# Kernel optimization log

Measured on AMD Instinct MI355X. Metric: run time of the kernel, lower is better.

## Reference

```python
import jax, jax.numpy as jnp
import numpy as np

B, C_IN, H, W = 8, 32, 64, 64
C = 64  # num_channels


def setup_inputs() -> dict:
    key = jax.random.key(0)
    ks = jax.random.split(key, 9)
    s_in = 1.0 / np.sqrt(C_IN)
    s_c = 1.0 / np.sqrt(C)
    return {
        "x": jax.random.normal(ks[0], (B, C_IN, H, W), dtype=jnp.float32),
        "wq": jax.random.uniform(ks[1], (C, C_IN), jnp.float32, -s_in, s_in),
        "bq": jax.random.uniform(ks[2], (C,), jnp.float32, -s_in, s_in),
        "wk": jax.random.uniform(ks[3], (C, C_IN), jnp.float32, -s_in, s_in),
        "bk": jax.random.uniform(ks[4], (C,), jnp.float32, -s_in, s_in),
        "wv": jax.random.uniform(ks[5], (C, C_IN), jnp.float32, -s_in, s_in),
        "bv": jax.random.uniform(ks[6], (C,), jnp.float32, -s_in, s_in),
        "wo": jax.random.uniform(ks[7], (C_IN, C), jnp.float32, -s_c, s_c),
        "bo": jax.random.uniform(ks[8], (C_IN,), jnp.float32, -s_c, s_c),
    }


def reference(x, wq, bq, wk, bk, wv, bv, wo, bo):
    b, c_in, h, w = x.shape
    n = h * w
    # 1x1 convs == per-pixel linear projections; produce (B, N, C) directly
    q = (jnp.einsum('bchw,oc->bhwo', x, wq) + bq).reshape(b, n, -1)
    k = (jnp.einsum('bchw,oc->bhwo', x, wk) + bk).reshape(b, n, -1)
    v = (jnp.einsum('bchw,oc->bhwo', x, wv) + bv).reshape(b, n, -1)
    # unscaled attention over spatial positions (no 1/sqrt(d) in original)
    scores = jnp.einsum('bnc,bmc->bnm', q, k)  # (B, N, N)
    attn = jax.nn.softmax(scores, axis=-1)
    out = jnp.einsum('bnm,bmc->bnc', attn, v)  # (B, N, C)
    out = out.reshape(b, h, w, -1)
    out = jnp.einsum('bhwc,oc->bohw', out, wo) + bo[None, :, None, None]
    return out + x
```

## Files before the change

### kernel.cpp

```cpp
#include <hip/hip_runtime.h>
#include <hip/hip_bf16.h>

#define CIN    32
#define NPIX   4096
#define DIM    64
#define LOG2E  1.4426950408889634f

#if __has_builtin(__builtin_amdgcn_exp2f)
#define EXP2(x) __builtin_amdgcn_exp2f(x)
#else
#define EXP2(x) exp2f(x)
#endif

typedef float  f32x4 __attribute__((ext_vector_type(4)));
typedef short  s16x8 __attribute__((ext_vector_type(8)));

__device__ __forceinline__ unsigned short bf16_bits(float f) {
    union { __hip_bfloat16 h; unsigned short u; } cv;
    cv.h = __float2bfloat16(f);
    return cv.u;
}


__global__ __launch_bounds__(256) void qkv_proj(
    const float* __restrict__ x,
    const float* __restrict__ wq, const float* __restrict__ bq,
    const float* __restrict__ wk, const float* __restrict__ bk,
    const float* __restrict__ wv, const float* __restrict__ bv,
    __hip_bfloat16* __restrict__ qb, __hip_bfloat16* __restrict__ kb,
    __hip_bfloat16* __restrict__ vb)
{
    __shared__ float Xs[CIN][64];
    __shared__ float wT[3][CIN][DIM];

    const int tid = threadIdx.x;
    const int b   = blockIdx.y;
    const int bx  = blockIdx.x;
    const int n0  = bx * 64;

    for (int i = tid; i < 3 * CIN * DIM; i += 256) {
        int m = i >> 11, r = i & 2047, c = r >> 6, o = r & 63;
        const float* wsrc = (m == 0) ? wq : (m == 1) ? wk : wv;
        float wv0 = wsrc[o * CIN + c];
        wT[m][c][o] = (m == 0) ? wv0 * LOG2E : wv0;
    }
    for (int i = tid * 4; i < CIN * 64; i += 1024) {
        int c = i >> 6, p = i & 63;
        *(f32x4*)&Xs[c][p] = *(const f32x4*)&x[((size_t)b * CIN + c) * NPIX + n0 + p];
    }
    __syncthreads();

    const int w    = tid >> 6;
    const int lane = tid & 63;
    const int l16  = lane >> 2;
    const int quad = lane & 3;

    const int T  = bx * 4 + w;
    const int px = T * 16 + l16;

    float aq[2][8], ak[2][8];
    #pragma unroll
    for (int kb2 = 0; kb2 < 2; kb2++) {
        f32x4 bq0 = *(const f32x4*)&bq[kb2 * 32 + quad * 8];
        f32x4 bq1 = *(const f32x4*)&bq[kb2 * 32 + quad * 8 + 4];
        f32x4 bk0 = *(const f32x4*)&bk[kb2 * 32 + quad * 8];
        f32x4 bk1 = *(const f32x4*)&bk[kb2 * 32 + quad * 8 + 4];
        #pragma unroll
        for (int j = 0; j < 4; j++) {
            aq[kb2][j] = bq0[j] * LOG2E; aq[kb2][j + 4] = bq1[j] * LOG2E;
            ak[kb2][j] = bk0[j];         ak[kb2][j + 4] = bk1[j];
        }
    }
    #pragma unroll 8
    for (int c = 0; c < CIN; c++) {
        const float xc = Xs[c][w * 16 + l16];
        #pragma unroll
        for (int kb2 = 0; kb2 < 2; kb2++) {
            f32x4 q0 = *(const f32x4*)&wT[0][c][kb2 * 32 + quad * 8];
            f32x4 q1 = *(const f32x4*)&wT[0][c][kb2 * 32 + quad * 8 + 4];
            f32x4 k0 = *(const f32x4*)&wT[1][c][kb2 * 32 + quad * 8];
            f32x4 k1 = *(const f32x4*)&wT[1][c][kb2 * 32 + quad * 8 + 4];
            #pragma unroll
            for (int j = 0; j < 4; j++) {
                aq[kb2][j]     += xc * q0[j];
                aq[kb2][j + 4] += xc * q1[j];
                ak[kb2][j]     += xc * k0[j];
                ak[kb2][j + 4] += xc * k1[j];
            }
        }
    }
    #pragma unroll
    for (int kb2 = 0; kb2 < 2; kb2++) {
        union { s16x8 v; __hip_bfloat16 h[8]; } pq, pk;
        #pragma unroll
        for (int j = 0; j < 8; j++) {
            pq.h[j] = __float2bfloat16(aq[kb2][j]);
            pk.h[j] = __float2bfloat16(ak[kb2][j]);
        }
        *(s16x8*)(qb + ((size_t)b * NPIX + px) * DIM + kb2 * 32 + quad * 8) = pq.v;
        const size_t koff =
            ((((size_t)(b * 256 + T) * 2 + kb2) * 16 + l16) * 4 + quad) * 8;
        *(s16x8*)(kb + koff) = pk.v;
    }

    const int ch = w * 16 + l16;
    float av[2][8];
    {
        const float bvc = bv[ch];
        #pragma unroll
        for (int kh = 0; kh < 2; kh++)
            #pragma unroll
            for (int j = 0; j < 8; j++) av[kh][j] = bvc;
    }
    #pragma unroll 8
    for (int c = 0; c < CIN; c++) {
        const float wvc = wT[2][c][ch];
        f32x4 x0 = *(const f32x4*)&Xs[c][quad * 8];
        f32x4 x1 = *(const f32x4*)&Xs[c][quad * 8 + 4];
        f32x4 x2 = *(const f32x4*)&Xs[c][32 + quad * 8];
        f32x4 x3 = *(const f32x4*)&Xs[c][32 + quad * 8 + 4];
        #pragma unroll
        for (int j = 0; j < 4; j++) {
            av[0][j]     += x0[j] * wvc;
            av[0][j + 4] += x1[j] * wvc;
            av[1][j]     += x2[j] * wvc;
            av[1][j + 4] += x3[j] * wvc;
        }
    }
    #pragma unroll
    for (int kh = 0; kh < 2; kh++) {
        union { s16x8 v; __hip_bfloat16 h[8]; } pv;
        #pragma unroll
        for (int j = 0; j < 8; j++) pv.h[j] = __float2bfloat16(av[kh][j]);
        const size_t voff =
            (((((size_t)(b * 64 + bx) * 2 + kh) * 4 + w) * 16 + l16) * 4 + quad) * 8;
        *(s16x8*)(vb + voff) = pv.v;
    }
}

#define PM_OFF   0
#define RED_OFF  0
#define ON_OFF   51456
#define SMEM_SZ  60672

__global__ __launch_bounds__(256, 2) void attn_fused(
    const __hip_bfloat16* __restrict__ qb,
    const __hip_bfloat16* __restrict__ kbf,
    const __hip_bfloat16* __restrict__ vbf,
    const float* __restrict__ wo, const float* __restrict__ bo,
    const float* __restrict__ x, float* __restrict__ y)
{
    __shared__ __align__(16) char smem[SMEM_SZ];

    const int tid  = threadIdx.x;
    const int kq   = tid >> 6;
    const int lane = tid & 63;
    const int quad = lane >> 4, l16 = lane & 15;
    const int b    = blockIdx.x;
    const int row0 = blockIdx.y * 64;

    s16x8 qf[4][2];
    #pragma unroll
    for (int mt = 0; mt < 4; mt++)
        #pragma unroll
        for (int kb2 = 0; kb2 < 2; kb2++)
            qf[mt][kb2] = *(const s16x8*)(qb
                + ((size_t)b * NPIX + row0 + mt * 16 + l16) * DIM + kb2 * 32 + quad * 8);

    const f32x4 zero4 = {0.f, 0.f, 0.f, 0.f};
    f32x4 o[4][4];
    #pragma unroll
    for (int mt = 0; mt < 4; mt++)
        #pragma unroll
        for (int ct = 0; ct < 4; ct++) o[mt][ct] = zero4;
    f32x4 ol[4] = {zero4, zero4, zero4, zero4};

    s16x8 ones;
    #pragma unroll
    for (int j = 0; j < 8; j++) ones[j] = (short)0x3F80;

    const char* kp = (const char*)kbf + (size_t)b * 524288 + kq * 131072
                     + (l16 * 4 + quad) * 16;
    const char* vp = (const char*)vbf + (size_t)b * 524288 + kq * 131072
                     + (l16 * 4 + quad) * 16;
    char* pmw = smem + PM_OFF + kq * 4608;

    s16x8 ckA[4], ckB[4], cvf[4], pf[4];
    f32x4 st[2][4];

    auto compute_st = [&](s16x8 (&curK)[4]) {
        #pragma unroll
        for (int nt = 0; nt < 2; nt++)
            #pragma unroll
            for (int mt = 0; mt < 4; mt++) {
                st[nt][mt] = __builtin_amdgcn_mfma_f32_16x16x32_bf16(
                    curK[nt * 2 + 0], qf[mt][0], zero4, 0, 0, 0);
                st[nt][mt] = __builtin_amdgcn_mfma_f32_16x16x32_bf16(
                    curK[nt * 2 + 1], qf[mt][1], st[nt][mt], 0, 0, 0);
            }
    };
    auto load_k = [&](s16x8 (&dst)[4], int it) {
        #pragma unroll
        for (int i = 0; i < 4; i++)
            dst[i] = *(const s16x8*)(kp + (size_t)it * 4096 + i * 1024);
    };
    auto load_v = [&](int it) {
        #pragma unroll
        for (int i = 0; i < 4; i++)
            cvf[i] = *(const s16x8*)(vp + (size_t)it * 4096 + i * 1024);
    };
    auto pack_write = [&]() {
        #pragma unroll
        for (int nt = 0; nt < 2; nt++)
            #pragma unroll
            for (int mt = 0; mt < 4; mt++) {
                f32x4 p = st[nt][mt];
                #pragma unroll
                for (int r = 0; r < 4; r++) p[r] = EXP2(p[r]);
                unsigned int d0 = (__float_as_uint(p[1]) & 0xffff0000u)
                                | (__float_as_uint(p[0]) >> 16);
                unsigned int d1 = (__float_as_uint(p[3]) & 0xffff0000u)
                                | (__float_as_uint(p[2]) >> 16);
                unsigned long long dd = ((unsigned long long)d1 << 32) | d0;
                *(unsigned long long*)(pmw + (mt * 16 + l16) * 72 + nt * 32 + quad * 8) = dd;
            }
    };
    auto read_pf = [&]() {
        #pragma unroll
        for (int mt = 0; mt < 4; mt++)
            pf[mt] = *(const s16x8*)(pmw + (mt * 16 + l16) * 72 + quad * 16);
    };
    auto do_pv = [&]() {
        #pragma unroll
        for (int ct = 0; ct < 4; ct++)
            #pragma unroll
            for (int mt = 0; mt < 4; mt++)
                o[mt][ct] = __builtin_amdgcn_mfma_f32_16x16x32_bf16(
                    pf[mt], cvf[ct], o[mt][ct], 0, 0, 0);
        #pragma unroll
        for (int mt = 0; mt < 4; mt++)
            ol[mt] = __builtin_amdgcn_mfma_f32_16x16x32_bf16(
                pf[mt], ones, ol[mt], 0, 0, 0);
    };

    auto step = [&](s16x8 (&curK)[4], s16x8 (&nxtK)[4], int it) {
        compute_st(curK);
        load_k(nxtK, it + 1);
        do_pv();
        pack_write();
        read_pf();
        load_v(it);
    };

    load_k(ckA, 0);
    load_v(0);
    compute_st(ckA);
    load_k(ckB, 1);
    pack_write();
    read_pf();

    for (int it = 1; it < 31; it += 2) {
        step(ckB, ckA, it);
        step(ckA, ckB, it + 1);
    }
    step(ckB, ckA, 31);
    do_pv();

    __syncthreads();

    float* RED = (float*)(smem + RED_OFF);

    if (kq != 0) {
        float* R = RED + (kq - 1) * 64 * 66;
        #pragma unroll
        for (int mt = 0; mt < 4; mt++) {
            #pragma unroll
            for (int ct = 0; ct < 4; ct++)
                #pragma unroll
                for (int r = 0; r < 4; r++)
                    R[(mt * 16 + quad * 4 + r) * 66 + ct * 16 + l16] = o[mt][ct][r];
            if (l16 == 0)
                #pragma unroll
                for (int r = 0; r < 4; r++)
                    R[(mt * 16 + quad * 4 + r) * 66 + 64] = ol[mt][r];
        }
    }
    __syncthreads();

    if (kq == 0) {
        #pragma unroll
        for (int reg = 0; reg < 3; reg++) {
            const float* R = RED + reg * 64 * 66;
            #pragma unroll
            for (int mt = 0; mt < 4; mt++)
                #pragma unroll
                for (int r = 0; r < 4; r++) {
                    ol[mt][r] += R[(mt * 16 + quad * 4 + r) * 66 + 64];
                    #pragma unroll
                    for (int ct = 0; ct < 4; ct++)
                        o[mt][ct][r] += R[(mt * 16 + quad * 4 + r) * 66 + ct * 16 + l16];
                }
        }

        __hip_bfloat16* ON = (__hip_bfloat16*)(smem + ON_OFF);
        #pragma unroll
        for (int mt = 0; mt < 4; mt++)
            #pragma unroll
            for (int r = 0; r < 4; r++) {
                const float inv = 1.0f / ol[mt][r];
                #pragma unroll
                for (int ct = 0; ct < 4; ct++)
                    ON[(mt * 16 + quad * 4 + r) * 72 + ct * 16 + l16]
                        = __float2bfloat16(o[mt][ct][r] * inv);
            }
        s16x8 af[4][2];
        #pragma unroll
        for (int mt = 0; mt < 4; mt++)
            #pragma unroll
            for (int kb2 = 0; kb2 < 2; kb2++)
                af[mt][kb2] = *(const s16x8*)(ON + (mt * 16 + l16) * 72
                                              + kb2 * 32 + quad * 8);

        f32x4 d[4][2];
        #pragma unroll
        for (int mt = 0; mt < 4; mt++)
            #pragma unroll
            for (int nt = 0; nt < 2; nt++) d[mt][nt] = zero4;
        #pragma unroll
        for (int nt = 0; nt < 2; nt++)
            #pragma unroll
            for (int kb2 = 0; kb2 < 2; kb2++) {
                const float* wp = wo + (size_t)(nt * 16 + l16) * DIM + kb2 * 32 + quad * 8;
                union { s16x8 v; __hip_bfloat16 h[8]; } wf;
                #pragma unroll
                for (int j = 0; j < 8; j++) wf.h[j] = __float2bfloat16(wp[j]);
                #pragma unroll
                for (int mt = 0; mt < 4; mt++)
                    d[mt][nt] = __builtin_amdgcn_mfma_f32_16x16x32_bf16(
                        af[mt][kb2], wf.v, d[mt][nt], 0, 0, 0);
            }

        #pragma unroll
        for (int nt = 0; nt < 2; nt++) {
            const int out = nt * 16 + l16;
            const float bias = bo[out];
            #pragma unroll
            for (int mt = 0; mt < 4; mt++)
                #pragma unroll
                for (int r = 0; r < 4; r++) {
                    const int row = row0 + mt * 16 + quad * 4 + r;
                    const size_t xi = ((size_t)b * CIN + out) * NPIX + row;
                    y[xi] = d[mt][nt][r] + bias + x[xi];
                }
        }
    }
}

extern "C" void kernel_launch(void* const* d_in, const int* in_sizes, int n_in,
                              void* d_out, int out_size, void* d_ws, size_t ws_size,
                              hipStream_t stream)
{
    const float* x  = (const float*)d_in[0];
    const float* wq = (const float*)d_in[1];
    const float* bq = (const float*)d_in[2];
    const float* wk = (const float*)d_in[3];
    const float* bk = (const float*)d_in[4];
    const float* wv = (const float*)d_in[5];
    const float* bv = (const float*)d_in[6];
    const float* wo = (const float*)d_in[7];
    const float* bo = (const float*)d_in[8];
    float* y = (float*)d_out;

    char* ws = (char*)d_ws;
    __hip_bfloat16* qb = (__hip_bfloat16*)(ws);
    __hip_bfloat16* kb = (__hip_bfloat16*)(ws + (4u << 20));
    __hip_bfloat16* vb = (__hip_bfloat16*)(ws + (8u << 20));

    qkv_proj<<<dim3(64, 8), dim3(256), 0, stream>>>(x, wq, bq, wk, bk, wv, bv, qb, kb, vb);
    attn_fused<<<dim3(8, 64), dim3(256), 0, stream>>>(qb, kb, vb, wo, bo, x, y);
}
```

Before: 135.3 us.

## Split attention key loop across six waves and compute row sums on VALU

The fused attention block grows from 4 to 6 wavefronts (384 threads, launch bounds allowing 3 blocks per CU). Each wave handles about 21–22 of the 128 key tiles instead of 32, which shortens the serial key loop per wave. The softmax denominator is now summed in fp32 registers plus cross-lane shuffles instead of an extra MFMA against a vector of ones. The K double buffer becomes a single buffer, and the cross-wave reduction turns into a two-stage tree through shared memory with extra barriers. In exchange, register budget per thread tightens, loads and compute overlap less, and the row sum now uses unrounded fp32 values rather than the bf16 values fed to the P·V product.

After: 147.8 us. 9.2% more time.

```diff
diff --git a/kernel.cpp b/kernel.cpp
--- a/kernel.cpp
+++ b/kernel.cpp
@@ -140,10 +140,11 @@
 
 #define PM_OFF   0
 #define RED_OFF  0
-#define ON_OFF   51456
-#define SMEM_SZ  60672
-
-__global__ __launch_bounds__(256, 2) void attn_fused(
+#define LS_OFF   50688
+#define ON_OFF   50944
+#define SMEM_SZ  60160
+
+__global__ __launch_bounds__(384, 3) void attn_fused(
     const __hip_bfloat16* __restrict__ qb,
     const __hip_bfloat16* __restrict__ kbf,
     const __hip_bfloat16* __restrict__ vbf,
@@ -159,6 +160,9 @@
     const int b    = blockIdx.x;
     const int row0 = blockIdx.y * 64;
 
+    const int tstart = kq * 21 + (kq == 5 ? 1 : 0);
+    const int niter  = 21 + (kq >= 4 ? 1 : 0);
+
     s16x8 qf[4][2];
     #pragma unroll
     for (int mt = 0; mt < 4; mt++)
@@ -173,41 +177,35 @@
     for (int mt = 0; mt < 4; mt++)
         #pragma unroll
         for (int ct = 0; ct < 4; ct++) o[mt][ct] = zero4;
-    f32x4 ol[4] = {zero4, zero4, zero4, zero4};
-
-    s16x8 ones;
-    #pragma unroll
-    for (int j = 0; j < 8; j++) ones[j] = (short)0x3F80;
-
-    const char* kp = (const char*)kbf + (size_t)b * 524288 + kq * 131072
-                     + (l16 * 4 + quad) * 16;
-    const char* vp = (const char*)vbf + (size_t)b * 524288 + kq * 131072
-                     + (l16 * 4 + quad) * 16;
+    float l_lane[4] = {0.f, 0.f, 0.f, 0.f};
+
+    const char* kp0 = (const char*)kbf + (size_t)b * 524288 + (l16 * 4 + quad) * 16;
+    const char* vp0 = (const char*)vbf + (size_t)b * 524288 + (l16 * 4 + quad) * 16;
     char* pmw = smem + PM_OFF + kq * 4608;
 
-    s16x8 ckA[4], ckB[4], cvf[4], pf[4];
+    s16x8 ck[4], cvf[4], pf[4];
     f32x4 st[2][4];
 
-    auto compute_st = [&](s16x8 (&curK)[4]) {
+    auto compute_st = [&]() {
         #pragma unroll
         for (int nt = 0; nt < 2; nt++)
             #pragma unroll
             for (int mt = 0; mt < 4; mt++) {
                 st[nt][mt] = __builtin_amdgcn_mfma_f32_16x16x32_bf16(
-                    curK[nt * 2 + 0], qf[mt][0], zero4, 0, 0, 0);
+                    ck[nt * 2 + 0], qf[mt][0], zero4, 0, 0, 0);
                 st[nt][mt] = __builtin_amdgcn_mfma_f32_16x16x32_bf16(
-                    curK[nt * 2 + 1], qf[mt][1], st[nt][mt], 0, 0, 0);
-            }
-    };
-    auto load_k = [&](s16x8 (&dst)[4], int it) {
+                    ck[nt * 2 + 1], qf[mt][1], st[nt][mt], 0, 0, 0);
+            }
+    };
+    auto load_k = [&](int t) {
         #pragma unroll
         for (int i = 0; i < 4; i++)
-            dst[i] = *(const s16x8*)(kp + (size_t)it * 4096 + i * 1024);
-    };
-    auto load_v = [&](int it) {
+            ck[i] = *(const s16x8*)(kp0 + (size_t)t * 4096 + i * 1024);
+    };
+    auto load_v = [&](int t) {
         #pragma unroll
         for (int i = 0; i < 4; i++)
-            cvf[i] = *(const s16x8*)(vp + (size_t)it * 4096 + i * 1024);
+            cvf[i] = *(const s16x8*)(vp0 + (size_t)t * 4096 + i * 1024);
     };
     auto pack_write = [&]() {
         #pragma unroll
@@ -217,6 +215,7 @@
                 f32x4 p = st[nt][mt];
                 #pragma unroll
                 for (int r = 0; r < 4; r++) p[r] = EXP2(p[r]);
+                l_lane[mt] += (p[0] + p[1]) + (p[2] + p[3]);
                 unsigned int d0 = (__float_as_uint(p[1]) & 0xffff0000u)
                                 | (__float_as_uint(p[0]) >> 16);
                 unsigned int d1 = (__float_as_uint(p[3]) & 0xffff0000u)
@@ -237,41 +236,35 @@
             for (int mt = 0; mt < 4; mt++)
                 o[mt][ct] = __builtin_amdgcn_mfma_f32_16x16x32_bf16(
                     pf[mt], cvf[ct], o[mt][ct], 0, 0, 0);
-        #pragma unroll
-        for (int mt = 0; mt < 4; mt++)
-            ol[mt] = __builtin_amdgcn_mfma_f32_16x16x32_bf16(
-                pf[mt], ones, ol[mt], 0, 0, 0);
-    };
-
-    auto step = [&](s16x8 (&curK)[4], s16x8 (&nxtK)[4], int it) {
-        compute_st(curK);
-        load_k(nxtK, it + 1);
+    };
+
+    load_k(tstart);
+    load_v(tstart);
+    compute_st();
+    load_k(tstart + 1);
+    pack_write();
+    read_pf();
+
+    for (int it = tstart + 1; it < tstart + niter; it++) {
+        compute_st();
+        load_k(it + 1);
         do_pv();
         pack_write();
         read_pf();
         load_v(it);
-    };
-
-    load_k(ckA, 0);
-    load_v(0);
-    compute_st(ckA);
-    load_k(ckB, 1);
-    pack_write();
-    read_pf();
-
-    for (int it = 1; it < 31; it += 2) {
-        step(ckB, ckA, it);
-        step(ckA, ckB, it + 1);
-    }
-    step(ckB, ckA, 31);
+    }
     do_pv();
 
-    __syncthreads();
+    #pragma unroll
+    for (int mt = 0; mt < 4; mt++) {
+        l_lane[mt] += __shfl_xor(l_lane[mt], 16, 64);
+        l_lane[mt] += __shfl_xor(l_lane[mt], 32, 64);
+    }
 
     float* RED = (float*)(smem + RED_OFF);
 
-    if (kq != 0) {
-        float* R = RED + (kq - 1) * 64 * 66;
+    auto dump = [&](int bufid) {
+        float* R = RED + bufid * 64 * 66;
         #pragma unroll
         for (int mt = 0; mt < 4; mt++) {
             #pragma unroll
@@ -279,35 +272,46 @@
                 #pragma unroll
                 for (int r = 0; r < 4; r++)
                     R[(mt * 16 + quad * 4 + r) * 66 + ct * 16 + l16] = o[mt][ct][r];
-            if (l16 == 0)
-                #pragma unroll
-                for (int r = 0; r < 4; r++)
-                    R[(mt * 16 + quad * 4 + r) * 66 + 64] = ol[mt][r];
-        }
-    }
+            if (quad == 0)
+                R[(mt * 16 + l16) * 66 + 64] = l_lane[mt];
+        }
+    };
+    auto accum = [&](int bufid) {
+        const float* R = RED + bufid * 64 * 66;
+        #pragma unroll
+        for (int mt = 0; mt < 4; mt++) {
+            l_lane[mt] += R[(mt * 16 + l16) * 66 + 64];
+            #pragma unroll
+            for (int r = 0; r < 4; r++)
+                #pragma unroll
+                for (int ct = 0; ct < 4; ct++)
+                    o[mt][ct][r] += R[(mt * 16 + quad * 4 + r) * 66 + ct * 16 + l16];
+        }
+    };
+
+    __syncthreads();
+    if (kq >= 3) dump(kq - 3);
+    __syncthreads();
+    if (kq < 3) accum(kq);
+    __syncthreads();
+    if (kq == 1 || kq == 2) dump(kq - 1);
     __syncthreads();
 
     if (kq == 0) {
-        #pragma unroll
-        for (int reg = 0; reg < 3; reg++) {
-            const float* R = RED + reg * 64 * 66;
-            #pragma unroll
-            for (int mt = 0; mt < 4; mt++)
-                #pragma unroll
-                for (int r = 0; r < 4; r++) {
-                    ol[mt][r] += R[(mt * 16 + quad * 4 + r) * 66 + 64];
-                    #pragma unroll
-                    for (int ct = 0; ct < 4; ct++)
-                        o[mt][ct][r] += R[(mt * 16 + quad * 4 + r) * 66 + ct * 16 + l16];
-                }
-        }
+        accum(0);
+        accum(1);
+
+        float* LS = (float*)(smem + LS_OFF);
+        if (quad == 0)
+            #pragma unroll
+            for (int mt = 0; mt < 4; mt++) LS[mt * 16 + l16] = l_lane[mt];
 
         __hip_bfloat16* ON = (__hip_bfloat16*)(smem + ON_OFF);
         #pragma unroll
         for (int mt = 0; mt < 4; mt++)
             #pragma unroll
             for (int r = 0; r < 4; r++) {
-                const float inv = 1.0f / ol[mt][r];
+                const float inv = 1.0f / LS[mt * 16 + quad * 4 + r];
                 #pragma unroll
                 for (int ct = 0; ct < 4; ct++)
                     ON[(mt * 16 + quad * 4 + r) * 72 + ct * 16 + l16]
@@ -377,5 +381,5 @@
     __hip_bfloat16* vb = (__hip_bfloat16*)(ws + (8u << 20));
 
     qkv_proj<<<dim3(64, 8), dim3(256), 0, stream>>>(x, wq, bq, wk, bk, wv, bv, qb, kb, vb);
-    attn_fused<<<dim3(8, 64), dim3(256), 0, stream>>>(qb, kb, vb, wo, bo, x, y);
+    attn_fused<<<dim3(8, 64), dim3(384), 0, stream>>>(qb, kb, vb, wo, bo, x, y);
 }
```
